# Optimization experiments

Measured on AMD Instinct MI355X. Metric: run time of the kernel, lower is better.

Reference implementation:

```python
import jax, jax.numpy as jnp
import numpy as np
from jax import lax

EPS = 1e-5
NUM_GROUPS = 32
OFFSET_SCALE = 1.0
K = 3            # deformable conv kernel size
KK = K * K
DWK = 7          # depthwise kernel size for offset predictor


def group_norm(x, gamma, beta, num_groups=NUM_GROUPS):
    B, C, H, W = x.shape
    xg = x.reshape(B, num_groups, C // num_groups, H, W)
    m = xg.mean(axis=(2, 3, 4), keepdims=True)
    v = xg.var(axis=(2, 3, 4), keepdims=True)
    xn = ((xg - m) * lax.rsqrt(v + EPS)).reshape(B, C, H, W)
    return xn * gamma[None, :, None, None] + beta[None, :, None, None]


def bilinear_gather(x, py, px):
    # x: [B,C,H,W]; py, px: [B,KK,H,W] absolute sample coords -> [B,C,KK,H,W]
    B, C, H, W = x.shape
    y0 = jnp.floor(py)
    x0 = jnp.floor(px)
    wy1 = py - y0
    wx1 = px - x0
    wy0 = 1.0 - wy1
    wx0 = 1.0 - wx1
    xf = x.reshape(B, C, H * W)

    def gather(yi, xi):
        valid = (yi >= 0) & (yi <= H - 1) & (xi >= 0) & (xi <= W - 1)
        yc = jnp.clip(yi, 0, H - 1).astype(jnp.int32)
        xc = jnp.clip(xi, 0, W - 1).astype(jnp.int32)
        idx = (yc * W + xc).reshape(B, -1)                      # [B, KK*H*W]
        g = jax.vmap(lambda a, i: a[:, i])(xf, idx)             # [B, C, KK*H*W]
        g = g.reshape(B, C, KK, H, W)
        return g * valid.astype(x.dtype)[:, None]

    out = (gather(y0, x0) * (wy0 * wx0)[:, None]
           + gather(y0, x0 + 1.0) * (wy0 * wx1)[:, None]
           + gather(y0 + 1.0, x0) * (wy1 * wx0)[:, None]
           + gather(y0 + 1.0, x0 + 1.0) * (wy1 * wx1)[:, None])
    return out


def deform_conv(x, dw, pw, pwb, w, b):
    # x: [B,C,H,W]; dw: [C,1,DWK,DWK] depthwise; pw: [2*KK,C,1,1]; w: [O,C,K,K]
    B, C, H, W = x.shape
    dn = ('NCHW', 'OIHW', 'NCHW')
    f = lax.conv_general_dilated(x, dw, (1, 1), 'SAME',
                                 feature_group_count=C, dimension_numbers=dn)
    off = lax.conv_general_dilated(f, pw, (1, 1), 'SAME', dimension_numbers=dn)
    off = (off + pwb[None, :, None, None]) * OFFSET_SCALE       # [B,2*KK,H,W]
    off = off.reshape(B, KK, 2, H, W)
    ks = jnp.arange(K, dtype=x.dtype) - (K - 1) / 2             # [-1,0,1]
    ky = jnp.repeat(ks, K)                                      # [KK]
    kx = jnp.tile(ks, K)
    yy, xx = jnp.meshgrid(jnp.arange(H, dtype=x.dtype),
                          jnp.arange(W, dtype=x.dtype), indexing='ij')
    py = yy[None, None] + ky[None, :, None, None] + off[:, :, 0]  # [B,KK,H,W]
    px = xx[None, None] + kx[None, :, None, None] + off[:, :, 1]
    sampled = bilinear_gather(x, py, px)                        # [B,C,KK,H,W]
    O = w.shape[0]
    out = jnp.einsum('bckhw,ock->bohw', sampled, w.reshape(O, C, KK))
    return out + b[None, :, None, None]


def setup_inputs() -> dict:
    key = jax.random.key(0)
    ks = jax.random.split(key, 10)
    B, C, H, W = 4, 256, 64, 64
    O = C
    x = jax.random.normal(ks[0], (B, C, H, W), dtype=jnp.float32)

    def conv_w(k, shape, fan_in):
        return jax.random.normal(k, shape, dtype=jnp.float32) / np.sqrt(fan_in)

    inp = {
        'x': x,
        'gn1_g': jnp.ones((C,), jnp.float32), 'gn1_b': jnp.zeros((C,), jnp.float32),
        'dw1': conv_w(ks[1], (C, 1, DWK, DWK), DWK * DWK),
        'pw1': jax.random.normal(ks[2], (2 * KK, C, 1, 1), jnp.float32) * 0.01,
        'pwb1': jnp.zeros((2 * KK,), jnp.float32),
        'w1': conv_w(ks[3], (O, C, K, K), C * KK),
        'b1': jnp.zeros((O,), jnp.float32),
        'gn2_g': jnp.ones((O,), jnp.float32), 'gn2_b': jnp.zeros((O,), jnp.float32),
        'dw2': conv_w(ks[4], (O, 1, DWK, DWK), DWK * DWK),
        'pw2': jax.random.normal(ks[5], (2 * KK, O, 1, 1), jnp.float32) * 0.01,
        'pwb2': jnp.zeros((2 * KK,), jnp.float32),
        'w2': conv_w(ks[6], (O, O, K, K), O * KK),
        'b2': jnp.zeros((O,), jnp.float32),
    }
    return inp


def reference(x, gn1_g, gn1_b, dw1, pw1, pwb1, w1, b1,
              gn2_g, gn2_b, dw2, pw2, pwb2, w2, b2):
    h = jax.nn.relu(group_norm(x, gn1_g, gn1_b))
    h = deform_conv(h, dw1, pw1, pwb1, w1, b1)
    h = jax.nn.relu(group_norm(h, gn2_g, gn2_b))
    # Dropout / DropPath are identity in eval mode
    h = deform_conv(h, dw2, pw2, pwb2, w2, b2)
    return h + x  # shortcut is Identity (in_channels == out_channels)
```

## Files before the change

### kernel.cpp

```cpp
#include <hip/hip_runtime.h>

#define B_    4
#define C_    256
#define H_    64
#define W_    64
#define HW_   4096
#define NG_   32
#define CPG_  8
#define KK_   9
#define NOFF_ 18

typedef __attribute__((ext_vector_type(8))) short short8;
typedef __attribute__((ext_vector_type(4))) short short4v;
typedef __attribute__((ext_vector_type(4))) float floatx4;
typedef __attribute__((ext_vector_type(16))) float floatx16;

static __device__ __forceinline__ short f2bf(float f) {
    union { float f; unsigned u; } v; v.f = f;
    unsigned r = v.u + 0x7fff + ((v.u >> 16) & 1);
    return (short)(r >> 16);
}
static __device__ __forceinline__ float bf2f(short s) {
    union { unsigned u; float f; } v;
    v.u = ((unsigned)(unsigned short)s) << 16;
    return v.f;
}
static __device__ __forceinline__ unsigned pkbf(float lo, float hi) {
    unsigned r;
    asm("v_cvt_pk_bf16_f32 %0, %1, %2" : "=v"(r) : "v"(lo), "v"(hi));
    return r;
}

__global__ __launch_bounds__(1024) void gn_relu_f32_kernel(
    const float* __restrict__ in, const float* __restrict__ gamma,
    const float* __restrict__ beta, short* __restrict__ outb)
{
    int b = blockIdx.x >> 5;
    int g = blockIdx.x & 31;
    const int N = CPG_ * HW_;
    size_t base = ((size_t)(b * C_ + g * CPG_)) * HW_;
    const float4* in4 = (const float4*)(in + base);
    int t = threadIdx.x;

    float s = 0.f, ss = 0.f;
    for (int i = t; i < N / 4; i += 1024) {
        float4 v = in4[i];
        s  += v.x + v.y + v.z + v.w;
        ss += v.x * v.x + v.y * v.y + v.z * v.z + v.w * v.w;
    }
    #pragma unroll
    for (int off = 32; off > 0; off >>= 1) {
        s  += __shfl_down(s, off, 64);
        ss += __shfl_down(ss, off, 64);
    }
    __shared__ float red[32];
    __shared__ float sh_rs, sh_m;
    int wid = t >> 6;
    if ((t & 63) == 0) { red[wid] = s; red[16 + wid] = ss; }
    __syncthreads();
    if (t == 0) {
        float S = 0.f, SS = 0.f;
        #pragma unroll
        for (int i = 0; i < 16; ++i) { S += red[i]; SS += red[16 + i]; }
        float m = S / (float)N;
        float var = SS / (float)N - m * m;
        sh_rs = rsqrtf(var + 1e-5f);
        sh_m = m;
    }
    __syncthreads();
    float rs = sh_rs, m = sh_m;
    short4v* out4 = (short4v*)(outb + base);
    for (int i = t; i < N / 4; i += 1024) {
        int ch = g * CPG_ + (i >> 10);
        float ga = gamma[ch] * rs;
        float be = beta[ch] - m * ga;
        float4 v = in4[i];
        short4v o;
        o.x = f2bf(fmaxf(fmaf(v.x, ga, be), 0.f));
        o.y = f2bf(fmaxf(fmaf(v.y, ga, be), 0.f));
        o.z = f2bf(fmaxf(fmaf(v.z, ga, be), 0.f));
        o.w = f2bf(fmaxf(fmaf(v.w, ga, be), 0.f));
        out4[i] = o;
    }
}

__global__ __launch_bounds__(1024) void gn_relu_bf16_kernel(
    const short* __restrict__ in, const float* __restrict__ gamma,
    const float* __restrict__ beta, short* __restrict__ outb)
{
    int b = blockIdx.x >> 5;
    int g = blockIdx.x & 31;
    const int N = CPG_ * HW_;
    size_t base = ((size_t)(b * C_ + g * CPG_)) * HW_;
    const short4v* in4 = (const short4v*)(in + base);
    int t = threadIdx.x;

    float s = 0.f, ss = 0.f;
    for (int i = t; i < N / 4; i += 1024) {
        short4v sv = in4[i];
        float vx = bf2f(sv.x), vy = bf2f(sv.y), vz = bf2f(sv.z), vw = bf2f(sv.w);
        s  += vx + vy + vz + vw;
        ss += vx * vx + vy * vy + vz * vz + vw * vw;
    }
    #pragma unroll
    for (int off = 32; off > 0; off >>= 1) {
        s  += __shfl_down(s, off, 64);
        ss += __shfl_down(ss, off, 64);
    }
    __shared__ float red[32];
    __shared__ float sh_rs, sh_m;
    int wid = t >> 6;
    if ((t & 63) == 0) { red[wid] = s; red[16 + wid] = ss; }
    __syncthreads();
    if (t == 0) {
        float S = 0.f, SS = 0.f;
        #pragma unroll
        for (int i = 0; i < 16; ++i) { S += red[i]; SS += red[16 + i]; }
        float m = S / (float)N;
        float var = SS / (float)N - m * m;
        sh_rs = rsqrtf(var + 1e-5f);
        sh_m = m;
    }
    __syncthreads();
    float rs = sh_rs, m = sh_m;
    short4v* out4 = (short4v*)(outb + base);
    for (int i = t; i < N / 4; i += 1024) {
        int ch = g * CPG_ + (i >> 10);
        float ga = gamma[ch] * rs;
        float be = beta[ch] - m * ga;
        short4v sv = in4[i];
        short4v o;
        o.x = f2bf(fmaxf(fmaf(bf2f(sv.x), ga, be), 0.f));
        o.y = f2bf(fmaxf(fmaf(bf2f(sv.y), ga, be), 0.f));
        o.z = f2bf(fmaxf(fmaf(bf2f(sv.z), ga, be), 0.f));
        o.w = f2bf(fmaxf(fmaf(bf2f(sv.w), ga, be), 0.f));
        out4[i] = o;
    }
}

__global__ __launch_bounds__(256) void dw7t_tr_kernel(
    const short* __restrict__ in,
    const float* __restrict__ dwk,
    short* __restrict__ fdwt,
    short* __restrict__ ht)
{
    __shared__ __align__(16) char smem[78112];
    int t = threadIdx.x;
    int blk = blockIdx.x;
    if (blk < 256) {
        short (*tile)[38][72] = (short(*)[38][72])smem;
        float (*wk8)[49]      = (float(*)[49])(smem + 43776);
        short (*outs)[2048]   = (short(*)[2048])(smem + 45344);
        int b = blk >> 6, o8 = (blk >> 1) & 31, rh = blk & 1;
        int c0 = o8 * 8;
        unsigned* tz = (unsigned*)smem;
        for (int i = t; i < 10944; i += 256) tz[i] = 0u;
        for (int i = t; i < 392; i += 256)
            wk8[i / 49][i % 49] = dwk[(c0 + i / 49) * 49 + (i % 49)];
        __syncthreads();
        for (int ch = 0; ch < 8; ++ch) {
            const short* src = in + ((size_t)(b * C_ + c0 + ch)) * HW_;
            for (int i = t; i < 608; i += 256) {
                int rr = i >> 4, xq = i & 15;
                int ry = rh * 32 + rr - 3;
                if (ry >= 0 && ry < 64) {
                    short4v v = *(const short4v*)(src + ry * 64 + xq * 4);
                    *(short4v*)&tile[ch][rr][4 + xq * 4] = v;
                }
            }
        }
        __syncthreads();
        for (int it = 0; it < 16; ++it) {
            int q = it * 256 + t;
            int ch = q >> 9, y = (q >> 4) & 31, x0 = (q & 15) << 2;
            float a0 = 0.f, a1 = 0.f, a2 = 0.f, a3 = 0.f;
            const float* wr0 = wk8[ch];
            #pragma unroll
            for (int dy = 0; dy < 7; ++dy) {
                const short* trw = &tile[ch][y + dy][x0];
                short4v s0 = *(const short4v*)trw;
                short4v s1 = *(const short4v*)(trw + 4);
                short4v s2 = *(const short4v*)(trw + 8);
                float r[12] = {bf2f(s0.x), bf2f(s0.y), bf2f(s0.z), bf2f(s0.w),
                               bf2f(s1.x), bf2f(s1.y), bf2f(s1.z), bf2f(s1.w),
                               bf2f(s2.x), bf2f(s2.y), bf2f(s2.z), bf2f(s2.w)};
                const float* wr = wr0 + dy * 7;
                #pragma unroll
                for (int dx = 0; dx < 7; ++dx) {
                    float wv = wr[dx];
                    a0 = fmaf(r[dx + 1], wv, a0);
                    a1 = fmaf(r[dx + 2], wv, a1);
                    a2 = fmaf(r[dx + 3], wv, a2);
                    a3 = fmaf(r[dx + 4], wv, a3);
                }
            }
            short4v o;
            o.x = f2bf(a0); o.y = f2bf(a1); o.z = f2bf(a2); o.w = f2bf(a3);
            *(short4v*)&outs[ch][y * 64 + x0] = o;
        }
        __syncthreads();
        for (int it = 0; it < 8; ++it) {
            int p = it * 256 + t;
            short8 v;
            #pragma unroll
            for (int ch = 0; ch < 8; ++ch) v[ch] = outs[ch][p];
            *(short8*)(fdwt + (((size_t)(b * 64 + rh * 32 + (p >> 6)) * 32 + o8) * 64
                               + (p & 63)) * 8) = v;
        }
    } else {
        unsigned* ltile = (unsigned*)smem;
        int q0 = blk - 256;
        int q = ((q0 & 7) << 5) | (q0 >> 3);
        int b = q >> 6;
        int px0 = (q & 63) * 64;
        const short* sb = in + (size_t)b * C_ * HW_;
        int pq4 = t & 15, cphi = t >> 4;
        #pragma unroll
        for (int i = 0; i < 8; ++i) {
            int cp = i * 16 + cphi;
            const short* r0 = sb + (size_t)(2 * cp) * HW_ + px0 + pq4 * 4;
            short4v lo = *(const short4v*)r0;
            short4v hi = *(const short4v*)(r0 + HW_);
            #pragma unroll
            for (int j = 0; j < 4; ++j) {
                int pl = pq4 * 4 + j;
                unsigned wrd = (unsigned)(unsigned short)lo[j]
                             | ((unsigned)(unsigned short)hi[j] << 16);
                ltile[pl * 132 + (cp ^ ((pl & 7) << 2))] = wrd;
            }
        }
        __syncthreads();
        int co = t & 31, ph2 = t >> 5;
        #pragma unroll
        for (int r = 0; r < 8; ++r) {
            int pl = r * 8 + ph2;
            uint4 v = *(const uint4*)&ltile[pl * 132 + ((co * 4) ^ ((pl & 7) << 2))];
            *(uint4*)(ht + ((size_t)b * HW_ + px0 + pl) * C_ + co * 8) = v;
        }
    }
}

__global__ __launch_bounds__(256) void wpack_all_kernel(
    const float* __restrict__ w1, const float* __restrict__ w2,
    const float* __restrict__ pw1, const float* __restrict__ pw2,
    short* __restrict__ wp1, short* __restrict__ wp2,
    short* __restrict__ ppk1, short* __restrict__ ppk2)
{
    int blk = blockIdx.x;
    if (blk < 4608) {
        const float* w = (blk < 2304) ? w1 : w2;
        short* wp = (blk < 2304) ? wp1 : wp2;
        int src = (blk % 2304) * 256 + threadIdx.x;
        float v = w[src];
        int o = src / (C_ * KK_);
        int r = src - o * (C_ * KK_);
        int c = r / KK_;
        int g = r - c * KK_;
        int ot   = o >> 5;
        int lane = (o & 31) | (((c >> 3) & 1) << 5);
        int j    = c & 7;
        int slab = g * 16 + (c >> 4);
        wp[(slab << 12) | (ot << 9) | (lane << 3) | j] = f2bf(v);
    } else {
        int q = blk - 4608;
        const float* pw = (q < 32) ? pw1 : pw2;
        short* ppk = (q < 32) ? ppk1 : ppk2;
        int idx = (q & 31) * 256 + threadIdx.x;
        int j = idx & 7, lane = (idx >> 3) & 63;
        int ot = (idx >> 9) & 1, sl = idx >> 10;
        int o = ot * 16 + (lane & 15);
        int k = sl * 32 + (lane >> 4) * 8 + j;
        ppk[idx] = (o < NOFF_) ? f2bf(pw[o * C_ + k]) : (short)0;
    }
}

__global__ __launch_bounds__(1024, 4) void deform_fused_kernel(
    const short* __restrict__ ht,   const short* __restrict__ fdw,
    const short* __restrict__ ppk,  const float* __restrict__ pwb,
    const short* __restrict__ wp,   const float* __restrict__ bias,
    const float* __restrict__ resid, float* __restrict__ outf,
    short* __restrict__ outb)
{
    int lb = ((blockIdx.x & 7) << 5) | (blockIdx.x >> 3);
    int b = lb >> 6;
    int row = lb & 63;
    __shared__ int   i00[576], i01[576], i10[576], i11[576];
    __shared__ float c00[576], c01[576], c10[576], c11[576];
    __shared__ __align__(16) short sbuf[2][2][8192];
    float* off_lds = (float*)&sbuf[0][0][0];
    int t = threadIdx.x;
    int wv = t >> 6, lane = t & 63;
    int pq = lane >> 4, pr = lane & 15;
    int l31 = lane & 31, hi = lane >> 5;

    if (wv < 8) {
        int ot = wv & 1, ptw = wv >> 1;
        int px = ptw * 16 + pr;
        const short8* fdw8 = (const short8*)fdw;
        size_t fbase = ((size_t)(b * 64 + row)) * 32;
        const short8* ap = (const short8*)ppk;
        floatx4 pacc = (floatx4){0.f, 0.f, 0.f, 0.f};
        #pragma unroll
        for (int sl = 0; sl < 8; ++sl) {
            short8 af = ap[(sl * 2 + ot) * 64 + lane];
            short8 bf = fdw8[(fbase + sl * 4 + pq) * 64 + px];
            pacc = __builtin_amdgcn_mfma_f32_16x16x32_bf16(af, bf, pacc, 0, 0, 0);
        }
        #pragma unroll
        for (int r = 0; r < 4; ++r) {
            int o = ot * 16 + pq * 4 + r;
            if (o < NOFF_) off_lds[o * 64 + px] = pacc[r] + pwb[o];
        }
    }
    __syncthreads();

    if (t < 576) {
        int e = t;
        int k = e >> 6, p = e & 63;
        float offy = off_lds[(2 * k) * 64 + p];
        float offx = off_lds[(2 * k + 1) * 64 + p];
        float py = (float)row + (float)(k / 3 - 1) + offy;
        float px = (float)p   + (float)(k % 3 - 1) + offx;
        float y0f = floorf(py), x0f = floorf(px);
        float wy1 = py - y0f, wx1 = px - x0f;
        float wy0 = 1.f - wy1, wx0 = 1.f - wx1;
        float y1f = y0f + 1.f, x1f = x0f + 1.f;
        bool vy0 = (y0f >= 0.f) && (y0f <= 63.f);
        bool vy1 = (y1f >= 0.f) && (y1f <= 63.f);
        bool vx0 = (x0f >= 0.f) && (x0f <= 63.f);
        bool vx1 = (x1f >= 0.f) && (x1f <= 63.f);
        int iy0 = (int)fminf(fmaxf(y0f, 0.f), 63.f);
        int iy1 = (int)fminf(fmaxf(y1f, 0.f), 63.f);
        int ix0 = (int)fminf(fmaxf(x0f, 0.f), 63.f);
        int ix1 = (int)fminf(fmaxf(x1f, 0.f), 63.f);
        i00[e] = iy0 * 64 + ix0; i01[e] = iy0 * 64 + ix1;
        i10[e] = iy1 * 64 + ix0; i11[e] = iy1 * 64 + ix1;
        c00[e] = (vy0 && vx0) ? wy0 * wx0 : 0.f;
        c01[e] = (vy0 && vx1) ? wy0 * wx1 : 0.f;
        c10[e] = (vy1 && vx0) ? wy1 * wx0 : 0.f;
        c11[e] = (vy1 && vx1) ? wy1 * wx1 : 0.f;
    }
    __syncthreads();

    int c8a = t & 7;
    int pan = (t >> 3) & 1;
    int spx = t >> 4;
    const short* hb0 = ht + ((size_t)b * HW_) * C_ + pan * 128 + c8a * 8;
    const short* hb1 = hb0 + 64;
    int slotA = (c8a ^ (spx & 15)) * 8;
    int slotB = ((c8a + 8) ^ (spx & 15)) * 8;
    int srow = spx * 128;

    short8 ra[4], rb[4];
    auto prefetch = [&](int g) {
        int e = g * 64 + spx;
        int a00 = i00[e], a01 = i01[e], a10 = i10[e], a11 = i11[e];
        ra[0] = *(const short8*)(hb0 + (size_t)a00 * C_);
        ra[1] = *(const short8*)(hb0 + (size_t)a01 * C_);
        ra[2] = *(const short8*)(hb0 + (size_t)a10 * C_);
        ra[3] = *(const short8*)(hb0 + (size_t)a11 * C_);
        rb[0] = *(const short8*)(hb1 + (size_t)a00 * C_);
        rb[1] = *(const short8*)(hb1 + (size_t)a01 * C_);
        rb[2] = *(const short8*)(hb1 + (size_t)a10 * C_);
        rb[3] = *(const short8*)(hb1 + (size_t)a11 * C_);
    };
    auto stage_write = [&](int g, int bi) {
        int e = g * 64 + spx;
        float w00 = c00[e], w01 = c01[e], w10 = c10[e], w11 = c11[e];
        uint4 va, vb;
        float f0, f1;
        #define BLEND(R, J) (w00 * bf2f(R[0][J]) + w01 * bf2f(R[1][J]) \
                           + w10 * bf2f(R[2][J]) + w11 * bf2f(R[3][J]))
        f0 = BLEND(ra, 0); f1 = BLEND(ra, 1); va.x = pkbf(f0, f1);
        f0 = BLEND(ra, 2); f1 = BLEND(ra, 3); va.y = pkbf(f0, f1);
        f0 = BLEND(ra, 4); f1 = BLEND(ra, 5); va.z = pkbf(f0, f1);
        f0 = BLEND(ra, 6); f1 = BLEND(ra, 7); va.w = pkbf(f0, f1);
        f0 = BLEND(rb, 0); f1 = BLEND(rb, 1); vb.x = pkbf(f0, f1);
        f0 = BLEND(rb, 2); f1 = BLEND(rb, 3); vb.y = pkbf(f0, f1);
        f0 = BLEND(rb, 4); f1 = BLEND(rb, 5); vb.z = pkbf(f0, f1);
        f0 = BLEND(rb, 6); f1 = BLEND(rb, 7); vb.w = pkbf(f0, f1);
        #undef BLEND
        short* sp = &sbuf[bi][pan][srow];
        *(uint4*)&sp[slotA] = va;
        *(uint4*)&sp[slotB] = vb;
    };

    int pairId = wv & 7;
    int half = wv >> 3;

    floatx16 acc[2];
    #pragma unroll
    for (int i = 0; i < 16; ++i) { acc[0][i] = 0.f; acc[1][i] = 0.f; }

    prefetch(0);
    stage_write(0, 0);
    prefetch(1);
    __syncthreads();

    const short8* wp8 = (const short8*)wp;
    int msk = l31 & 15;

    for (int g = 0; g < 9; ++g) {
        const short* sb = &sbuf[g & 1][half][0];
        short8 af[8];
        #pragma unroll
        for (int q = 0; q < 8; ++q)
            af[q] = wp8[(size_t)(((g * 16 + half * 8 + q) * 8 + pairId) * 64 + lane)];
        #pragma unroll
        for (int q = 0; q < 8; ++q) {
            int so = ((((q << 1) | hi) ^ msk) << 3);
            short8 b0 = *(const short8*)&sb[l31 * 128 + so];
            short8 b1 = *(const short8*)&sb[(32 + l31) * 128 + so];
            acc[0] = __builtin_amdgcn_mfma_f32_32x32x16_bf16(af[q], b0, acc[0], 0, 0, 0);
            acc[1] = __builtin_amdgcn_mfma_f32_32x32x16_bf16(af[q], b1, acc[1], 0, 0, 0);
        }
        if (g + 1 < 9) {
            stage_write(g + 1, (g + 1) & 1);
            if (g + 2 < 9) prefetch(g + 2);
        }
        __syncthreads();
    }

    float* xch = (float*)&sbuf[0][0][0];
    int wreg = (pairId * 2 + half) * 1024;
    floatx16 aw = half ? acc[0] : acc[1];
    floatx4* xq = (floatx4*)xch;
    #pragma unroll
    for (int j = 0; j < 4; ++j) {
        floatx4 v = {aw[j * 4 + 0], aw[j * 4 + 1], aw[j * 4 + 2], aw[j * 4 + 3]};
        xq[(wreg >> 2) + j * 64 + lane] = v;
    }
    __syncthreads();
    int rreg = (pairId * 2 + (half ^ 1)) * 1024;
    floatx16 ac = half ? acc[1] : acc[0];
    #pragma unroll
    for (int j = 0; j < 4; ++j) {
        floatx4 v = xq[(rreg >> 2) + j * 64 + lane];
        ac[j * 4 + 0] += v.x; ac[j * 4 + 1] += v.y;
        ac[j * 4 + 2] += v.z; ac[j * 4 + 3] += v.w;
    }

    #pragma unroll
    for (int r = 0; r < 16; ++r) {
        int o = pairId * 32 + (r & 3) + 8 * (r >> 2) + 4 * hi;
        float v = ac[r] + bias[o];
        size_t ob = ((size_t)(b * C_ + o)) * HW_ + row * 64 + half * 32 + l31;
        if (outf) {
            if (resid) v += resid[ob];
            outf[ob] = v;
        } else {
            outb[ob] = f2bf(v);
        }
    }
}

extern "C" void kernel_launch(void* const* d_in, const int* in_sizes, int n_in,
                              void* d_out, int out_size, void* d_ws, size_t ws_size,
                              hipStream_t stream)
{
    const float* x     = (const float*)d_in[0];
    const float* gn1_g = (const float*)d_in[1];
    const float* gn1_b = (const float*)d_in[2];
    const float* dw1   = (const float*)d_in[3];
    const float* pw1   = (const float*)d_in[4];
    const float* pwb1  = (const float*)d_in[5];
    const float* w1    = (const float*)d_in[6];
    const float* b1    = (const float*)d_in[7];
    const float* gn2_g = (const float*)d_in[8];
    const float* gn2_b = (const float*)d_in[9];
    const float* dw2   = (const float*)d_in[10];
    const float* pw2   = (const float*)d_in[11];
    const float* pwb2  = (const float*)d_in[12];
    const float* w2    = (const float*)d_in[13];
    const float* b2    = (const float*)d_in[14];
    float* out = (float*)d_out;

    float* ws   = (float*)d_ws;
    short* y1b  = (short*)ws;
    short* hbf  = (short*)(ws + 2097152);
    short* hbt  = (short*)(ws + 4194304);
    short* fdwt = (short*)(ws + 8388608);
    short* wp1  = (short*)(ws + 10485760);
    short* wp2  = (short*)(ws + 10780672);
    short* ppk1 = (short*)(ws + 11075584);
    short* ppk2 = (short*)(ws + 11079680);

    wpack_all_kernel<<<4672, 256, 0, stream>>>(w1, w2, pw1, pw2,
                                               wp1, wp2, ppk1, ppk2);

    gn_relu_f32_kernel<<<B_ * NG_, 1024, 0, stream>>>(x, gn1_g, gn1_b, hbf);
    dw7t_tr_kernel<<<512, 256, 0, stream>>>(hbf, dw1, fdwt, hbt);
    deform_fused_kernel<<<B_ * H_, 1024, 0, stream>>>(
        hbt, fdwt, ppk1, pwb1, wp1, b1, nullptr, nullptr, y1b);

    gn_relu_bf16_kernel<<<B_ * NG_, 1024, 0, stream>>>(y1b, gn2_g, gn2_b, hbf);
    dw7t_tr_kernel<<<512, 256, 0, stream>>>(hbf, dw2, fdwt, hbt);
    deform_fused_kernel<<<B_ * H_, 1024, 0, stream>>>(
        hbt, fdwt, ppk2, pwb2, wp2, b2, x, out, nullptr);
}
```

Before: 269.6 us.

## Warp-specialize deformable conv: producer waves gather, consumer waves run MFMA

```diff
diff --git a/kernel.cpp b/kernel.cpp
--- a/kernel.cpp
+++ b/kernel.cpp
@@ -342,114 +342,118 @@
     }
     __syncthreads();
 
-    int c8a = t & 7;
-    int pan = (t >> 3) & 1;
-    int spx = t >> 4;
-    const short* hb0 = ht + ((size_t)b * HW_) * C_ + pan * 128 + c8a * 8;
-    const short* hb1 = hb0 + 64;
-    int slotA = (c8a ^ (spx & 15)) * 8;
-    int slotB = ((c8a + 8) ^ (spx & 15)) * 8;
-    int srow = spx * 128;
-
-    short8 ra[4], rb[4];
-    auto prefetch = [&](int g) {
-        int e = g * 64 + spx;
+    int msk = l31 & 15;
+
+    const short8* wp8 = (const short8*)wp;
+    floatx16 acc0, acc1;
+    #pragma unroll
+    for (int i = 0; i < 16; ++i) { acc0[i] = 0.f; acc1[i] = 0.f; }
+
+    int tp = t & 511;
+    int pj = tp & 7;
+    int psx = tp >> 3;
+    const short* base = ht + ((size_t)b * HW_) * C_;
+    const short* pb0 = base + pj * 8;
+    const short* pb1 = pb0 + 64;
+    const short* pb2 = base + 128 + pj * 8;
+    const short* pb3 = pb2 + 64;
+    int sl0 = (pj ^ (psx & 15)) * 8;
+    int sl1 = ((pj + 8) ^ (psx & 15)) * 8;
+    int psrow = psx * 128;
+
+    auto pstage = [&](int g, int bi) {
+        int e = g * 64 + psx;
         int a00 = i00[e], a01 = i01[e], a10 = i10[e], a11 = i11[e];
-        ra[0] = *(const short8*)(hb0 + (size_t)a00 * C_);
-        ra[1] = *(const short8*)(hb0 + (size_t)a01 * C_);
-        ra[2] = *(const short8*)(hb0 + (size_t)a10 * C_);
-        ra[3] = *(const short8*)(hb0 + (size_t)a11 * C_);
-        rb[0] = *(const short8*)(hb1 + (size_t)a00 * C_);
-        rb[1] = *(const short8*)(hb1 + (size_t)a01 * C_);
-        rb[2] = *(const short8*)(hb1 + (size_t)a10 * C_);
-        rb[3] = *(const short8*)(hb1 + (size_t)a11 * C_);
-    };
-    auto stage_write = [&](int g, int bi) {
-        int e = g * 64 + spx;
         float w00 = c00[e], w01 = c01[e], w10 = c10[e], w11 = c11[e];
-        uint4 va, vb;
-        float f0, f1;
+        short8 r0[4], r1[4], r2[4], r3[4];
+        r0[0] = *(const short8*)(pb0 + (size_t)a00 * C_);
+        r0[1] = *(const short8*)(pb0 + (size_t)a01 * C_);
+        r0[2] = *(const short8*)(pb0 + (size_t)a10 * C_);
+        r0[3] = *(const short8*)(pb0 + (size_t)a11 * C_);
+        r1[0] = *(const short8*)(pb1 + (size_t)a00 * C_);
+        r1[1] = *(const short8*)(pb1 + (size_t)a01 * C_);
+        r1[2] = *(const short8*)(pb1 + (size_t)a10 * C_);
+        r1[3] = *(const short8*)(pb1 + (size_t)a11 * C_);
+        r2[0] = *(const short8*)(pb2 + (size_t)a00 * C_);
+        r2[1] = *(const short8*)(pb2 + (size_t)a01 * C_);
+        r2[2] = *(const short8*)(pb2 + (size_t)a10 * C_);
+        r2[3] = *(const short8*)(pb2 + (size_t)a11 * C_);
+        r3[0] = *(const short8*)(pb3 + (size_t)a00 * C_);
+        r3[1] = *(const short8*)(pb3 + (size_t)a01 * C_);
+        r3[2] = *(const short8*)(pb3 + (size_t)a10 * C_);
+        r3[3] = *(const short8*)(pb3 + (size_t)a11 * C_);
         #define BLEND(R, J) (w00 * bf2f(R[0][J]) + w01 * bf2f(R[1][J]) \
                            + w10 * bf2f(R[2][J]) + w11 * bf2f(R[3][J]))
-        f0 = BLEND(ra, 0); f1 = BLEND(ra, 1); va.x = pkbf(f0, f1);
-        f0 = BLEND(ra, 2); f1 = BLEND(ra, 3); va.y = pkbf(f0, f1);
-        f0 = BLEND(ra, 4); f1 = BLEND(ra, 5); va.z = pkbf(f0, f1);
-        f0 = BLEND(ra, 6); f1 = BLEND(ra, 7); va.w = pkbf(f0, f1);
-        f0 = BLEND(rb, 0); f1 = BLEND(rb, 1); vb.x = pkbf(f0, f1);
-        f0 = BLEND(rb, 2); f1 = BLEND(rb, 3); vb.y = pkbf(f0, f1);
-        f0 = BLEND(rb, 4); f1 = BLEND(rb, 5); vb.z = pkbf(f0, f1);
-        f0 = BLEND(rb, 6); f1 = BLEND(rb, 7); vb.w = pkbf(f0, f1);
+        uint4 v;
+        v.x = pkbf(BLEND(r0, 0), BLEND(r0, 1));
+        v.y = pkbf(BLEND(r0, 2), BLEND(r0, 3));
+        v.z = pkbf(BLEND(r0, 4), BLEND(r0, 5));
+        v.w = pkbf(BLEND(r0, 6), BLEND(r0, 7));
+        *(uint4*)&sbuf[bi][0][psrow + sl0] = v;
+        v.x = pkbf(BLEND(r1, 0), BLEND(r1, 1));
+        v.y = pkbf(BLEND(r1, 2), BLEND(r1, 3));
+        v.z = pkbf(BLEND(r1, 4), BLEND(r1, 5));
+        v.w = pkbf(BLEND(r1, 6), BLEND(r1, 7));
+        *(uint4*)&sbuf[bi][0][psrow + sl1] = v;
+        v.x = pkbf(BLEND(r2, 0), BLEND(r2, 1));
+        v.y = pkbf(BLEND(r2, 2), BLEND(r2, 3));
+        v.z = pkbf(BLEND(r2, 4), BLEND(r2, 5));
+        v.w = pkbf(BLEND(r2, 6), BLEND(r2, 7));
+        *(uint4*)&sbuf[bi][1][psrow + sl0] = v;
+        v.x = pkbf(BLEND(r3, 0), BLEND(r3, 1));
+        v.y = pkbf(BLEND(r3, 2), BLEND(r3, 3));
+        v.z = pkbf(BLEND(r3, 4), BLEND(r3, 5));
+        v.w = pkbf(BLEND(r3, 6), BLEND(r3, 7));
+        *(uint4*)&sbuf[bi][1][psrow + sl1] = v;
         #undef BLEND
-        short* sp = &sbuf[bi][pan][srow];
-        *(uint4*)&sp[slotA] = va;
-        *(uint4*)&sp[slotB] = vb;
     };
 
-    int pairId = wv & 7;
-    int half = wv >> 3;
-
-    floatx16 acc[2];
-    #pragma unroll
-    for (int i = 0; i < 16; ++i) { acc[0][i] = 0.f; acc[1][i] = 0.f; }
-
-    prefetch(0);
-    stage_write(0, 0);
-    prefetch(1);
-    __syncthreads();
-
-    const short8* wp8 = (const short8*)wp;
-    int msk = l31 & 15;
+    if (wv >= 8) pstage(0, 0);
+    __syncthreads();
 
     for (int g = 0; g < 9; ++g) {
-        const short* sb = &sbuf[g & 1][half][0];
-        short8 af[8];
-        #pragma unroll
-        for (int q = 0; q < 8; ++q)
-            af[q] = wp8[(size_t)(((g * 16 + half * 8 + q) * 8 + pairId) * 64 + lane)];
-        #pragma unroll
-        for (int q = 0; q < 8; ++q) {
-            int so = ((((q << 1) | hi) ^ msk) << 3);
-            short8 b0 = *(const short8*)&sb[l31 * 128 + so];
-            short8 b1 = *(const short8*)&sb[(32 + l31) * 128 + so];
-            acc[0] = __builtin_amdgcn_mfma_f32_32x32x16_bf16(af[q], b0, acc[0], 0, 0, 0);
-            acc[1] = __builtin_amdgcn_mfma_f32_32x32x16_bf16(af[q], b1, acc[1], 0, 0, 0);
-        }
-        if (g + 1 < 9) {
-            stage_write(g + 1, (g + 1) & 1);
-            if (g + 2 < 9) prefetch(g + 2);
+        if (wv < 8) {
+            const short* sb0 = &sbuf[g & 1][0][0];
+            const short* sb1 = &sbuf[g & 1][1][0];
+            #pragma unroll
+            for (int bb = 0; bb < 4; ++bb) {
+                short8 af[4];
+                #pragma unroll
+                for (int q = 0; q < 4; ++q)
+                    af[q] = wp8[(size_t)(((g * 16 + bb * 4 + q) * 8 + wv) * 64 + lane)];
+                #pragma unroll
+                for (int q = 0; q < 4; ++q) {
+                    int s = bb * 4 + q;
+                    const short* sbp = (s < 8) ? sb0 : sb1;
+                    int so = ((((s & 7) * 2 + hi) ^ msk) << 3);
+                    short8 b0 = *(const short8*)&sbp[l31 * 128 + so];
+                    short8 b1 = *(const short8*)&sbp[(32 + l31) * 128 + so];
+                    acc0 = __builtin_amdgcn_mfma_f32_32x32x16_bf16(af[q], b0, acc0, 0, 0, 0);
+                    acc1 = __builtin_amdgcn_mfma_f32_32x32x16_bf16(af[q], b1, acc1, 0, 0, 0);
+                }
+            }
+        } else {
+            if (g + 1 < 9) pstage(g + 1, (g + 1) & 1);
         }
         __syncthreads();
     }
 
-    float* xch = (float*)&sbuf[0][0][0];
-    int wreg = (pairId * 2 + half) * 1024;
-    floatx16 aw = half ? acc[0] : acc[1];
-    floatx4* xq = (floatx4*)xch;
-    #pragma unroll
-    for (int j = 0; j < 4; ++j) {
-        floatx4 v = {aw[j * 4 + 0], aw[j * 4 + 1], aw[j * 4 + 2], aw[j * 4 + 3]};
-        xq[(wreg >> 2) + j * 64 + lane] = v;
-    }
-    __syncthreads();
-    int rreg = (pairId * 2 + (half ^ 1)) * 1024;
-    floatx16 ac = half ? acc[1] : acc[0];
-    #pragma unroll
-    for (int j = 0; j < 4; ++j) {
-        floatx4 v = xq[(rreg >> 2) + j * 64 + lane];
-        ac[j * 4 + 0] += v.x; ac[j * 4 + 1] += v.y;
-        ac[j * 4 + 2] += v.z; ac[j * 4 + 3] += v.w;
-    }
-
-    #pragma unroll
-    for (int r = 0; r < 16; ++r) {
-        int o = pairId * 32 + (r & 3) + 8 * (r >> 2) + 4 * hi;
-        float v = ac[r] + bias[o];
-        size_t ob = ((size_t)(b * C_ + o)) * HW_ + row * 64 + half * 32 + l31;
-        if (outf) {
-            if (resid) v += resid[ob];
-            outf[ob] = v;
-        } else {
-            outb[ob] = f2bf(v);
+    if (wv < 8) {
+        #pragma unroll
+        for (int r = 0; r < 16; ++r) {
+            int o = wv * 32 + (r & 3) + 8 * (r >> 2) + 4 * hi;
+            float bo = bias[o];
+            float v0 = acc0[r] + bo;
+            float v1 = acc1[r] + bo;
+            size_t ob = ((size_t)(b * C_ + o)) * HW_ + row * 64 + l31;
+            if (outf) {
+                if (resid) { v0 += resid[ob]; v1 += resid[ob + 32]; }
+                outf[ob] = v0;
+                outf[ob + 32] = v1;
+            } else {
+                outb[ob] = f2bf(v0);
+                outb[ob + 32] = f2bf(v1);
+            }
         }
     }
 }
```

After: 254.3 us. -5.7%, faster.

## Fuse GroupNorm2 statistics into deform conv epilogue; cache GN1 input in LDS

Applied to the files above, without the earlier changes.

```diff
diff --git a/kernel.cpp b/kernel.cpp
--- a/kernel.cpp
+++ b/kernel.cpp
@@ -35,6 +35,9 @@
     const float* __restrict__ in, const float* __restrict__ gamma,
     const float* __restrict__ beta, short* __restrict__ outb)
 {
+    __shared__ float cache[32768];
+    __shared__ float red[32];
+    __shared__ float sh_rs, sh_m;
     int b = blockIdx.x >> 5;
     int g = blockIdx.x & 31;
     const int N = CPG_ * HW_;
@@ -45,6 +48,7 @@
     float s = 0.f, ss = 0.f;
     for (int i = t; i < N / 4; i += 1024) {
         float4 v = in4[i];
+        *(float4*)&cache[i * 4] = v;
         s  += v.x + v.y + v.z + v.w;
         ss += v.x * v.x + v.y * v.y + v.z * v.z + v.w * v.w;
     }
@@ -53,8 +57,6 @@
         s  += __shfl_down(s, off, 64);
         ss += __shfl_down(ss, off, 64);
     }
-    __shared__ float red[32];
-    __shared__ float sh_rs, sh_m;
     int wid = t >> 6;
     if ((t & 63) == 0) { red[wid] = s; red[16 + wid] = ss; }
     __syncthreads();
@@ -74,7 +76,7 @@
         int ch = g * CPG_ + (i >> 10);
         float ga = gamma[ch] * rs;
         float be = beta[ch] - m * ga;
-        float4 v = in4[i];
+        float4 v = *(const float4*)&cache[i * 4];
         short4v o;
         o.x = f2bf(fmaxf(fmaf(v.x, ga, be), 0.f));
         o.y = f2bf(fmaxf(fmaf(v.y, ga, be), 0.f));
@@ -84,47 +86,24 @@
     }
 }
 
-__global__ __launch_bounds__(1024) void gn_relu_bf16_kernel(
-    const short* __restrict__ in, const float* __restrict__ gamma,
-    const float* __restrict__ beta, short* __restrict__ outb)
+__global__ __launch_bounds__(1024) void gn_apply_bf16_kernel(
+    const short* __restrict__ in, const float* __restrict__ gstats,
+    const float* __restrict__ gamma, const float* __restrict__ beta,
+    short* __restrict__ outb)
 {
-    int b = blockIdx.x >> 5;
-    int g = blockIdx.x & 31;
-    const int N = CPG_ * HW_;
+    int blk = blockIdx.x;
+    int b = blk >> 7, g = (blk >> 2) & 31, qq = blk & 3;
+    const float Ninv = 1.f / (float)(CPG_ * HW_);
+    int sidx = b * 32 + g;
+    float m   = gstats[sidx] * Ninv;
+    float var = gstats[128 + sidx] * Ninv - m * m;
+    float rs  = rsqrtf(var + 1e-5f);
     size_t base = ((size_t)(b * C_ + g * CPG_)) * HW_;
     const short4v* in4 = (const short4v*)(in + base);
+    short4v* out4 = (short4v*)(outb + base);
     int t = threadIdx.x;
-
-    float s = 0.f, ss = 0.f;
-    for (int i = t; i < N / 4; i += 1024) {
-        short4v sv = in4[i];
-        float vx = bf2f(sv.x), vy = bf2f(sv.y), vz = bf2f(sv.z), vw = bf2f(sv.w);
-        s  += vx + vy + vz + vw;
-        ss += vx * vx + vy * vy + vz * vz + vw * vw;
-    }
-    #pragma unroll
-    for (int off = 32; off > 0; off >>= 1) {
-        s  += __shfl_down(s, off, 64);
-        ss += __shfl_down(ss, off, 64);
-    }
-    __shared__ float red[32];
-    __shared__ float sh_rs, sh_m;
-    int wid = t >> 6;
-    if ((t & 63) == 0) { red[wid] = s; red[16 + wid] = ss; }
-    __syncthreads();
-    if (t == 0) {
-        float S = 0.f, SS = 0.f;
-        #pragma unroll
-        for (int i = 0; i < 16; ++i) { S += red[i]; SS += red[16 + i]; }
-        float m = S / (float)N;
-        float var = SS / (float)N - m * m;
-        sh_rs = rsqrtf(var + 1e-5f);
-        sh_m = m;
-    }
-    __syncthreads();
-    float rs = sh_rs, m = sh_m;
-    short4v* out4 = (short4v*)(outb + base);
-    for (int i = t; i < N / 4; i += 1024) {
+    int i0 = qq * 2048;
+    for (int i = i0 + t; i < i0 + 2048; i += 1024) {
         int ch = g * CPG_ + (i >> 10);
         float ga = gamma[ch] * rs;
         float be = beta[ch] - m * ga;
@@ -279,7 +258,7 @@
     const short* __restrict__ ppk,  const float* __restrict__ pwb,
     const short* __restrict__ wp,   const float* __restrict__ bias,
     const float* __restrict__ resid, float* __restrict__ outf,
-    short* __restrict__ outb)
+    short* __restrict__ outb,       float* __restrict__ gstats)
 {
     int lb = ((blockIdx.x & 7) << 5) | (blockIdx.x >> 3);
     int b = lb >> 6;
@@ -287,6 +266,7 @@
     __shared__ int   i00[576], i01[576], i10[576], i11[576];
     __shared__ float c00[576], c01[576], c10[576], c11[576];
     __shared__ __align__(16) short sbuf[2][2][8192];
+    __shared__ float stat_lds[16][8];
     float* off_lds = (float*)&sbuf[0][0][0];
     int t = threadIdx.x;
     int wv = t >> 6, lane = t & 63;
@@ -402,17 +382,21 @@
 
     for (int g = 0; g < 9; ++g) {
         const short* sb = &sbuf[g & 1][half][0];
-        short8 af[8];
-        #pragma unroll
-        for (int q = 0; q < 8; ++q)
-            af[q] = wp8[(size_t)(((g * 16 + half * 8 + q) * 8 + pairId) * 64 + lane)];
-        #pragma unroll
-        for (int q = 0; q < 8; ++q) {
-            int so = ((((q << 1) | hi) ^ msk) << 3);
-            short8 b0 = *(const short8*)&sb[l31 * 128 + so];
-            short8 b1 = *(const short8*)&sb[(32 + l31) * 128 + so];
-            acc[0] = __builtin_amdgcn_mfma_f32_32x32x16_bf16(af[q], b0, acc[0], 0, 0, 0);
-            acc[1] = __builtin_amdgcn_mfma_f32_32x32x16_bf16(af[q], b1, acc[1], 0, 0, 0);
+        #pragma unroll
+        for (int q4 = 0; q4 < 2; ++q4) {
+            short8 af[4];
+            #pragma unroll
+            for (int qq = 0; qq < 4; ++qq)
+                af[qq] = wp8[(size_t)(((g * 16 + half * 8 + q4 * 4 + qq) * 8 + pairId) * 64 + lane)];
+            #pragma unroll
+            for (int qq = 0; qq < 4; ++qq) {
+                int ksl = q4 * 4 + qq;
+                int so = ((((ksl << 1) | hi) ^ msk) << 3);
+                short8 b0 = *(const short8*)&sb[l31 * 128 + so];
+                short8 b1 = *(const short8*)&sb[(32 + l31) * 128 + so];
+                acc[0] = __builtin_amdgcn_mfma_f32_32x32x16_bf16(af[qq], b0, acc[0], 0, 0, 0);
+                acc[1] = __builtin_amdgcn_mfma_f32_32x32x16_bf16(af[qq], b1, acc[1], 0, 0, 0);
+            }
         }
         if (g + 1 < 9) {
             stage_write(g + 1, (g + 1) & 1);
@@ -440,6 +424,8 @@
         ac[j * 4 + 2] += v.z; ac[j * 4 + 3] += v.w;
     }
 
+    float sj[4] = {0.f, 0.f, 0.f, 0.f};
+    float qj[4] = {0.f, 0.f, 0.f, 0.f};
     #pragma unroll
     for (int r = 0; r < 16; ++r) {
         int o = pairId * 32 + (r & 3) + 8 * (r >> 2) + 4 * hi;
@@ -450,6 +436,34 @@
             outf[ob] = v;
         } else {
             outb[ob] = f2bf(v);
+            sj[r >> 2] += v;
+            qj[r >> 2] += v * v;
+        }
+    }
+    if (gstats) {
+        #pragma unroll
+        for (int off = 32; off > 0; off >>= 1) {
+            #pragma unroll
+            for (int j = 0; j < 4; ++j) {
+                sj[j] += __shfl_down(sj[j], off, 64);
+                qj[j] += __shfl_down(qj[j], off, 64);
+            }
+        }
+        if (lane == 0) {
+            #pragma unroll
+            for (int j = 0; j < 4; ++j) {
+                stat_lds[wv][j] = sj[j];
+                stat_lds[wv][4 + j] = qj[j];
+            }
+        }
+        __syncthreads();
+        if (t < 32) {
+            int pid = t >> 2, j = t & 3;
+            float sT = stat_lds[pid][j] + stat_lds[pid + 8][j];
+            float qT = stat_lds[pid][4 + j] + stat_lds[pid + 8][4 + j];
+            int idx = b * 32 + pid * 4 + j;
+            atomicAdd(&gstats[idx], sT);
+            atomicAdd(&gstats[128 + idx], qT);
         }
     }
 }
@@ -484,17 +498,19 @@
     short* wp2  = (short*)(ws + 10780672);
     short* ppk1 = (short*)(ws + 11075584);
     short* ppk2 = (short*)(ws + 11079680);
+    float* gstats = ws + 11083776;
 
     wpack_all_kernel<<<4672, 256, 0, stream>>>(w1, w2, pw1, pw2,
                                                wp1, wp2, ppk1, ppk2);
+    hipMemsetAsync(gstats, 0, 256 * sizeof(float), stream);
 
     gn_relu_f32_kernel<<<B_ * NG_, 1024, 0, stream>>>(x, gn1_g, gn1_b, hbf);
     dw7t_tr_kernel<<<512, 256, 0, stream>>>(hbf, dw1, fdwt, hbt);
     deform_fused_kernel<<<B_ * H_, 1024, 0, stream>>>(
-        hbt, fdwt, ppk1, pwb1, wp1, b1, nullptr, nullptr, y1b);
-
-    gn_relu_bf16_kernel<<<B_ * NG_, 1024, 0, stream>>>(y1b, gn2_g, gn2_b, hbf);
+        hbt, fdwt, ppk1, pwb1, wp1, b1, nullptr, nullptr, y1b, gstats);
+
+    gn_apply_bf16_kernel<<<512, 1024, 0, stream>>>(y1b, gstats, gn2_g, gn2_b, hbf);
     dw7t_tr_kernel<<<512, 256, 0, stream>>>(hbf, dw2, fdwt, hbt);
     deform_fused_kernel<<<B_ * H_, 1024, 0, stream>>>(
-        hbt, fdwt, ppk2, pwb2, wp2, b2, x, out, nullptr);
-}
+        hbt, fdwt, ppk2, pwb2, wp2, b2, x, out, nullptr, nullptr);
+}
```

Measured after the change: 242.8 us. 10.0% less time.
